# Performance work log

Hardware: AMD Instinct MI355X
Metric: run time of the kernel (lower is better)

## Reference

```python
import jax, jax.numpy as jnp
import numpy as np

NB, NL, V, VOCAB, D, TOPK = 16, 64, 16384, 32000, 256, 16
NITER, EARLY, RW = 8, 2, 0.8


def setup_inputs():
    key = jax.random.key(0)
    ks = jax.random.split(key, 8)
    probas = jax.random.uniform(ks[0], (NB, NL, V), dtype=jnp.float32) + 1e-6
    h_d = jax.random.normal(ks[1], (NB, NL, D), dtype=jnp.float32)
    lengths = jax.random.randint(ks[2], (NB,), NL // 2, NL + 1)
    mask = (jnp.arange(NL)[None, :] < lengths[:, None]).astype(jnp.int32)  # prefix mask
    batch_vocab = jax.random.randint(ks[3], (V,), 0, VOCAB)
    emb_table = jax.random.normal(ks[4], (VOCAB, D), dtype=jnp.float32) * 0.02
    W1 = jax.random.normal(ks[5], (2 * D, D), dtype=jnp.float32) * 0.006
    b1 = jnp.zeros((D,), dtype=jnp.float32)
    return {"probas": probas, "h_d": h_d, "mask": mask, "batch_vocab": batch_vocab,
            "emb_table": emb_table, "W1": W1, "b1": b1}


def _forward(probas, h_d, mask, batch_vocab, emb_table, W1, b1):
    maskf = mask.astype(probas.dtype)
    MAP = jnp.argmax(probas, axis=-1)                       # [nb,nl]
    topk_vals, topk_idx = jax.lax.top_k(probas, TOPK)       # [nb,nl,K]
    topk_vals = jnp.where(mask[..., None] < 1, 1.0, topk_vals)
    logits = jnp.log(topk_vals)                             # Categorical(probs) == categorical(log p)
    sLens = jnp.sum(mask, axis=1)                           # [nb]
    one_hot = jnp.arange(NL)[None, :] == (sLens - 1)[:, None]  # one_hot_by_mask: last valid pos
    m2d = (mask[:, :, None] * mask[:, None, :]) > 0
    eyeM = jnp.eye(NL, dtype=probas.dtype)
    h_masked = h_d * maskf[..., None]

    def step(carry, k):
        max_score, best, count, stopped = carry
        choice = jax.random.categorical(k, logits)          # [nb,nl]
        samples = jnp.take_along_axis(topk_idx, choice[..., None], axis=-1)[..., 0]
        samples = jnp.where(one_hot, MAP, samples)
        embs = emb_table[batch_vocab[samples]] * maskf[..., None]   # gather+embed, masked
        new_embs = jax.nn.relu(jnp.concatenate([embs, h_masked], axis=-1) @ W1 + b1)
        Kmat = jnp.einsum('bld,bmd->blm', new_embs, new_embs)       # [nb,nl,nl]
        # det of leading lxl submatrix == det with padded rows/cols replaced by identity
        score = jnp.linalg.det(jnp.where(m2d, Kmat, eyeM))          # [nb]
        improved = score > max_score
        any_imp = jnp.any(improved)
        count = jnp.where(any_imp, 0, count + 1)
        upd = improved & (~stopped)
        stopped = stopped | ((~any_imp) & (count >= EARLY))
        max_score = jnp.where(upd, score, max_score)
        best = jnp.where(upd[:, None], samples, best)
        return (max_score, best, count, stopped), None

    init = (jnp.full((NB,), -jnp.inf, probas.dtype), MAP, jnp.int32(0), jnp.bool_(False))
    keys = jax.random.split(jax.random.key(42), NITER)
    (max_score, best, _, _), _ = jax.lax.scan(step, init, keys)

    # diverse_proba: scatter redist_weight at best choice, (1-rw) elsewhere, renormalize
    am = jnp.where(jnp.arange(V)[None, None, :] == best[:, :, None], RW, 1.0 - RW).astype(probas.dtype)
    x = probas * am
    nm = jnp.sum(x, axis=-1, keepdims=True)
    nm = jnp.where(maskf[..., None] == 0, 1e-10, nm)
    return x / nm, max_score


def reference(probas, h_d, mask, batch_vocab, emb_table, W1, b1):
    return _forward(probas, h_d, mask, batch_vocab, emb_table, W1, b1)
```

## Files before the change

### kernel.cpp

```cpp
#include <hip/hip_runtime.h>
#include <math.h>
#include <stdint.h>


#define TINYF 1.17549435082228750797e-38f

#define KMX(r, c) (((r) * 68) + ((c) ^ ((((r) >> 3) & 7) << 2)))

struct Keys16 { uint32_t k[16]; };

__host__ __device__ inline void tf2x32(uint32_t k0, uint32_t k1,
                                       uint32_t x0, uint32_t x1,
                                       uint32_t* o0, uint32_t* o1) {
  uint32_t ks2 = k0 ^ k1 ^ 0x1BD11BDAu;
  uint32_t ks[3] = {k0, k1, ks2};
  uint32_t v0 = x0 + k0, v1 = x1 + k1;
  const int R0[4] = {13, 15, 26, 6};
  const int R1[4] = {17, 29, 16, 24};
#pragma unroll
  for (int g = 0; g < 5; ++g) {
    const int* RR = (g & 1) ? R1 : R0;
#pragma unroll
    for (int r = 0; r < 4; ++r) {
      v0 += v1;
      v1 = (v1 << RR[r]) | (v1 >> (32 - RR[r]));
      v1 ^= v0;
    }
    v0 += ks[(g + 1) % 3];
    v1 += ks[(g + 2) % 3] + (uint32_t)(g + 1);
  }
  *o0 = v0; *o1 = v1;
}

__device__ inline float logf_ref(float x) { return (float)log((double)x); }

__device__ inline void wsync() {
  asm volatile("s_waitcnt lgkmcnt(0)" ::: "memory");
  __builtin_amdgcn_sched_barrier(0);
}

__device__ inline unsigned long long u64max(unsigned long long a,
                                            unsigned long long b) {
  return (a > b) ? a : b;
}

__global__ __launch_bounds__(256) void k_topk(const float* __restrict__ probas,
                                              const int* __restrict__ mask,
                                              int* __restrict__ topk_idx,
                                              float* __restrict__ logits,
                                              float* __restrict__ S) {
  int row = blockIdx.x;
  int t = threadIdx.x;
  const float* p = probas + (size_t)row * 16384;
  __shared__ unsigned long long lists[256][16];
  __shared__ float swsum[4];
  __shared__ int lcnt;
  unsigned long long* cand = &lists[0][0];

  cand[t] = 0ull;
  cand[t + 256] = 0ull;
  if (t == 0) lcnt = 0;
  __syncthreads();

  const uint32_t TB = 0x3F7E0000u;
  float sum = 0.f;
  const float4* p4 = (const float4*)p;
#pragma unroll 4
  for (int j = 0; j < 16; ++j) {
    float4 x = p4[t + j * 256];
    int v0 = (t + j * 256) * 4;
    uint32_t u0 = __float_as_uint(x.x), u1 = __float_as_uint(x.y);
    uint32_t u2 = __float_as_uint(x.z), u3 = __float_as_uint(x.w);
    sum += x.x; sum += x.y; sum += x.z; sum += x.w;
    uint32_t um = max(max(u0, u1), max(u2, u3));
    if (um >= TB) {
      if (u0 >= TB) { int s = atomicAdd(&lcnt, 1); if (s < 512)
          cand[s] = ((unsigned long long)u0 << 32) | (unsigned)(~(v0 + 0)); }
      if (u1 >= TB) { int s = atomicAdd(&lcnt, 1); if (s < 512)
          cand[s] = ((unsigned long long)u1 << 32) | (unsigned)(~(v0 + 1)); }
      if (u2 >= TB) { int s = atomicAdd(&lcnt, 1); if (s < 512)
          cand[s] = ((unsigned long long)u2 << 32) | (unsigned)(~(v0 + 2)); }
      if (u3 >= TB) { int s = atomicAdd(&lcnt, 1); if (s < 512)
          cand[s] = ((unsigned long long)u3 << 32) | (unsigned)(~(v0 + 3)); }
    }
  }
#pragma unroll
  for (int off = 32; off >= 1; off >>= 1) sum += __shfl_down(sum, off);
  if ((t & 63) == 0) swsum[t >> 6] = sum;
  __syncthreads();
  if (t == 0) S[row] = ((swsum[0] + swsum[1]) + swsum[2]) + swsum[3];

  int n = lcnt;
  if (n >= 16 && n <= 512) {
    if (t < 64) {
      unsigned long long c[8];
#pragma unroll
      for (int k = 0; k < 8; ++k) c[k] = cand[t + 64 * k];
      unsigned long long win = 0ull;
#pragma unroll
      for (int r = 0; r < 16; ++r) {
        unsigned long long m = c[0];
#pragma unroll
        for (int k = 1; k < 8; ++k) m = u64max(m, c[k]);
#pragma unroll
        for (int off = 32; off >= 1; off >>= 1) {
          unsigned long long o = __shfl_xor(m, off);
          m = u64max(m, o);
        }
        if (t == r) win = m;
#pragma unroll
        for (int k = 0; k < 8; ++k) if (c[k] == m) c[k] = 0ull;
      }
      if (t < 16) {
        int idx = (int)(~(unsigned)(win & 0xFFFFFFFFull));
        float val = __uint_as_float((unsigned)(win >> 32));
        topk_idx[row * 16 + t] = idx;
        logits[row * 16 + t] = (mask[row] == 0) ? 0.0f : logf_ref(val);
      }
    }
    return;
  }

  {
    unsigned long long loc[16];
#pragma unroll
    for (int q = 0; q < 16; ++q) loc[q] = 0ull;
    for (int j = 0; j < 64; ++j) {
      int v = t + j * 256;
      float x = p[v];
      unsigned long long key =
          ((unsigned long long)__float_as_uint(x) << 32) | (unsigned)(~v);
      if (key > loc[15]) {
        loc[15] = key;
#pragma unroll
        for (int q = 15; q > 0; --q) {
          if (loc[q] > loc[q - 1]) {
            unsigned long long tmp = loc[q]; loc[q] = loc[q - 1]; loc[q - 1] = tmp;
          }
        }
      }
    }
    __syncthreads();
#pragma unroll
    for (int q = 0; q < 16; ++q) lists[t][q] = loc[q];
    __syncthreads();
    for (int nl = 128; nl >= 1; nl >>= 1) {
      if (t < nl) {
        unsigned long long M[16];
        int ia = 0, ib = 0;
#pragma unroll
        for (int q = 0; q < 16; ++q) {
          unsigned long long av = lists[t][ia];
          unsigned long long bv = lists[t + nl][ib];
          if (av >= bv) { M[q] = av; ia++; } else { M[q] = bv; ib++; }
        }
#pragma unroll
        for (int q = 0; q < 16; ++q) lists[t][q] = M[q];
      }
      __syncthreads();
    }
    if (t < 16) {
      unsigned long long key = lists[0][t];
      int idx = (int)(~(unsigned)(key & 0xFFFFFFFFull));
      float val = __uint_as_float((unsigned)(key >> 32));
      topk_idx[row * 16 + t] = idx;
      logits[row * 16 + t] = (mask[row] == 0) ? 0.0f : logf_ref(val);
    }
  }
}

__global__ __launch_bounds__(256) void k_sample(Keys16 keys,
                                                const int* __restrict__ mask,
                                                const int* __restrict__ topk_idx,
                                                const float* __restrict__ logits,
                                                int* __restrict__ samples,
                                                int* __restrict__ choice) {
  int tid = blockIdx.x * 256 + threadIdx.x;
  int i = tid >> 10;
  int rbl = tid & 1023;
  int b = rbl >> 6;
  int l = rbl & 63;
  uint32_t k0 = keys.k[2 * i], k1 = keys.k[2 * i + 1];
  int sl = 0;
  for (int m = 0; m < 64; ++m) sl += mask[b * 64 + m];
  float bestv = 0.f; int bestk = 0;
#pragma unroll
  for (int k = 0; k < 16; ++k) {
    uint32_t j = (uint32_t)((b * 64 + l) * 16 + k);
    uint32_t y0, y1;
    tf2x32(k0, k1, 0u, j, &y0, &y1);
    uint32_t bits = y0 ^ y1;
    float f = __uint_as_float((bits >> 9) | 0x3f800000u) - 1.0f;
    float u = fmaxf(TINYF, f * 1.0f + TINYF);
    float t1 = logf_ref(u);
    float g = -logf_ref(-t1);
    float sv = g + logits[rbl * 16 + k];
    if (k == 0 || sv > bestv) { bestv = sv; bestk = k; }
  }
  int ce = (l == sl - 1) ? 0 : bestk;
  choice[tid] = ce;
  samples[tid] = topk_idx[rbl * 16 + ce];
}

__global__ __launch_bounds__(256) void k_ce(const int* __restrict__ topk_idx,
                                            const int* __restrict__ batch_vocab,
                                            const float* __restrict__ emb,
                                            const float* __restrict__ W1,
                                            const float* __restrict__ h_d,
                                            const float* __restrict__ b1,
                                            const int* __restrict__ mask,
                                            float* __restrict__ Eall) {
  int row = blockIdx.x;
  int t = threadIdx.x;
  __shared__ int rid[16];
  __shared__ float e[16][256];
  __shared__ float hl[256];
  float mkf = (float)mask[row];
  if (t < 16) rid[t] = batch_vocab[topk_idx[row * 16 + t]];
  hl[t] = h_d[(size_t)row * 256 + t] * mkf;
  __syncthreads();
#pragma unroll
  for (int k = 0; k < 16; ++k) e[k][t] = emb[(size_t)rid[k] * 256 + t];
  __syncthreads();
  float acch = 0.f;
  for (int j0 = 0; j0 < 256; j0 += 4) {
    float4 hv = *(const float4*)&hl[j0];
    float w0 = W1[(256 + j0 + 0) * 256 + t];
    float w1 = W1[(256 + j0 + 1) * 256 + t];
    float w2 = W1[(256 + j0 + 2) * 256 + t];
    float w3 = W1[(256 + j0 + 3) * 256 + t];
    acch = fmaf(hv.x, w0, acch);
    acch = fmaf(hv.y, w1, acch);
    acch = fmaf(hv.z, w2, acch);
    acch = fmaf(hv.w, w3, acch);
  }
  float acc[16];
#pragma unroll
  for (int k = 0; k < 16; ++k) acc[k] = 0.f;
  for (int j0 = 0; j0 < 256; j0 += 4) {
    float w0 = W1[(j0 + 0) * 256 + t];
    float w1 = W1[(j0 + 1) * 256 + t];
    float w2 = W1[(j0 + 2) * 256 + t];
    float w3 = W1[(j0 + 3) * 256 + t];
#pragma unroll
    for (int k = 0; k < 16; ++k) {
      float4 ev = *(const float4*)&e[k][j0];
      acc[k] = fmaf(ev.x, w0, acc[k]);
      acc[k] = fmaf(ev.y, w1, acc[k]);
      acc[k] = fmaf(ev.z, w2, acc[k]);
      acc[k] = fmaf(ev.w, w3, acc[k]);
    }
  }
  float b1v = b1[t];
#pragma unroll
  for (int k = 0; k < 16; ++k) {
    float val = fmaf(mkf, acc[k], acch) + b1v;
    Eall[((size_t)row * 16 + k) * 256 + t] = fmaxf(val, 0.0f);
  }
}

__global__ __launch_bounds__(256) void k_gram(const float* __restrict__ Eall,
                                              const int* __restrict__ mask,
                                              const int* __restrict__ choice,
                                              float* __restrict__ scores) {
  int blk = blockIdx.x;
  int i = blk >> 4, b = blk & 15;
  int t = threadIdx.x;
  __shared__ __align__(16) float Ett[64][68];
  __shared__ __align__(16) float KmF[64 * 68];
  __shared__ int ch[64];
  int mskv = 0;
  if (t < 64) {
    ch[t] = choice[i * 1024 + b * 64 + t];
    mskv = mask[b * 64 + t];
  }
  __syncthreads();
  int l = t & 63, wd = t >> 6;
  const float* eptr =
      Eall + ((size_t)((b * 64 + l) * 16 + ch[l])) * 256 + wd * 16;
  float acc[16];
#pragma unroll
  for (int q = 0; q < 16; ++q) acc[q] = 0.f;
  int tx = t & 15, ty = t >> 4;
  for (int dt = 0; dt < 4; ++dt) {
    const float* src = eptr + dt * 64;
    float4 v0 = *(const float4*)(src + 0);
    float4 v1 = *(const float4*)(src + 4);
    float4 v2 = *(const float4*)(src + 8);
    float4 v3 = *(const float4*)(src + 12);
    int d0 = wd * 16;
    Ett[d0 +  0][l] = v0.x; Ett[d0 +  1][l] = v0.y;
    Ett[d0 +  2][l] = v0.z; Ett[d0 +  3][l] = v0.w;
    Ett[d0 +  4][l] = v1.x; Ett[d0 +  5][l] = v1.y;
    Ett[d0 +  6][l] = v1.z; Ett[d0 +  7][l] = v1.w;
    Ett[d0 +  8][l] = v2.x; Ett[d0 +  9][l] = v2.y;
    Ett[d0 + 10][l] = v2.z; Ett[d0 + 11][l] = v2.w;
    Ett[d0 + 12][l] = v3.x; Ett[d0 + 13][l] = v3.y;
    Ett[d0 + 14][l] = v3.z; Ett[d0 + 15][l] = v3.w;
    __syncthreads();
#pragma unroll 4
    for (int dd = 0; dd < 64; ++dd) {
      float4 av4 = *(const float4*)&Ett[dd][tx * 4];
      float4 bv4 = *(const float4*)&Ett[dd][ty * 4];
      float avv[4] = {av4.x, av4.y, av4.z, av4.w};
      float bvv[4] = {bv4.x, bv4.y, bv4.z, bv4.w};
#pragma unroll
      for (int a2 = 0; a2 < 4; ++a2)
#pragma unroll
        for (int c2 = 0; c2 < 4; ++c2)
          acc[a2 * 4 + c2] = fmaf(avv[a2], bvv[c2], acc[a2 * 4 + c2]);
    }
    __syncthreads();
  }
#pragma unroll
  for (int a2 = 0; a2 < 4; ++a2)
#pragma unroll
    for (int c2 = 0; c2 < 4; ++c2)
      KmF[KMX(tx * 4 + a2, ty * 4 + c2)] = acc[a2 * 4 + c2];
  __syncthreads();
  if (t >= 64) return;

  unsigned long long bal = __ballot(mskv != 0);
  int L = __popcll(bal);

  float sdet = 1.f, ssign = 1.f;
  int pos = t;
  float curcol = KmF[KMX(t, 0)];

  for (int p = 0; p < L; ++p) {
    bool cnd = (pos >= p) && (pos < L);
    unsigned lo = (((unsigned)(63 - pos)) << 6) | (unsigned)t;
    unsigned long long key =
        cnd ? ((((unsigned long long)__float_as_uint(fabsf(curcol))) << 32) | lo)
            : 0ull;
#pragma unroll
    for (int off = 32; off >= 1; off >>= 1) {
      unsigned long long o = __shfl_xor(key, off);
      if (o > key) key = o;
    }
    int lane_rb = (int)(key & 63u);
    int pb = 63 - (int)((key >> 6) & 63u);
    float kpp = __shfl(curcol, lane_rb);
    sdet *= kpp;
    if (pb != p) ssign = -ssign;
    int np = pos;
    if (pos == p) np = pb;
    if (t == lane_rb) np = p;
    pos = np;
    bool active = (pos > p) && (pos < L);
    if (active) {
      float f = (kpp != 0.f) ? (curcol / kpp) : 0.f;
      float nf = -f;
      int c0 = (p + 1) & ~3;
      int sel = (p + 1) & 3;
      for (int c = c0; c < L; c += 4) {
        float4 pr = *(const float4*)&KmF[KMX(lane_rb, c)];
        float4 tr = *(float4*)&KmF[KMX(t, c)];
        tr.x = fmaf(nf, pr.x, tr.x);
        tr.y = fmaf(nf, pr.y, tr.y);
        tr.z = fmaf(nf, pr.z, tr.z);
        tr.w = fmaf(nf, pr.w, tr.w);
        *(float4*)&KmF[KMX(t, c)] = tr;
        if (c == c0) {
          curcol = (sel == 0) ? tr.x : (sel == 1) ? tr.y
                 : (sel == 2) ? tr.z : tr.w;
        }
      }
    }
    wsync();
  }
  if (t == 0) scores[i * 16 + b] = sdet * ssign;
}

__global__ void k_select(const float* __restrict__ scores,
                         int* __restrict__ win,
                         float* __restrict__ out_ms) {
  if (threadIdx.x == 0 && blockIdx.x == 0) {
    float ms[16]; int w[16];
    for (int b = 0; b < 16; ++b) { ms[b] = -INFINITY; w[b] = -1; }
    int count = 0; bool stopped = false;
    for (int i = 0; i < 8; ++i) {
      bool any = false; bool imp[16];
      for (int b = 0; b < 16; ++b) {
        imp[b] = scores[i * 16 + b] > ms[b];
        any = any || imp[b];
      }
      count = any ? 0 : (count + 1);
      for (int b = 0; b < 16; ++b) {
        if (imp[b] && !stopped) { ms[b] = scores[i * 16 + b]; w[b] = i; }
      }
      stopped = stopped || ((!any) && (count >= 2));
    }
    for (int b = 0; b < 16; ++b) { win[b] = w[b]; out_ms[b] = ms[b]; }
  }
}

__global__ __launch_bounds__(256) void k_out(const float* __restrict__ probas,
                                             const int* __restrict__ mask,
                                             const int* __restrict__ samples,
                                             const int* __restrict__ topk_idx,
                                             const int* __restrict__ win,
                                             const float* __restrict__ S,
                                             float* __restrict__ out) {
  int row = blockIdx.x;
  int b = row >> 6;
  int t = threadIdx.x;
  int wi = win[b];
  int best = (wi >= 0) ? samples[wi * 1024 + row] : topk_idx[row * 16];
  const float* p = probas + (size_t)row * 16384;
  float* o = out + (size_t)row * 16384;
  float nm;
  if (mask[row] == 0) {
    nm = 1e-10f;
  } else {
    nm = 0.2f * S[row] + 0.6f * p[best];
  }
  const float4* p4 = (const float4*)p;
  float4* o4 = (float4*)o;
  for (int f = t; f < 4096; f += 256) {
    float4 x = p4[f];
    int v0 = f << 2;
    float4 r;
    r.x = x.x * ((v0 + 0 == best) ? 0.8f : 0.2f) / nm;
    r.y = x.y * ((v0 + 1 == best) ? 0.8f : 0.2f) / nm;
    r.z = x.z * ((v0 + 2 == best) ? 0.8f : 0.2f) / nm;
    r.w = x.w * ((v0 + 3 == best) ? 0.8f : 0.2f) / nm;
    o4[f] = r;
  }
}

extern "C" void kernel_launch(void* const* d_in, const int* in_sizes, int n_in,
                              void* d_out, int out_size, void* d_ws, size_t ws_size,
                              hipStream_t stream) {
  const float* probas = (const float*)d_in[0];
  const float* h_d    = (const float*)d_in[1];
  const int*   mask   = (const int*)d_in[2];
  const int*   bvoc   = (const int*)d_in[3];
  const float* emb    = (const float*)d_in[4];
  const float* W1     = (const float*)d_in[5];
  const float* b1     = (const float*)d_in[6];
  float* out = (float*)d_out;

  char* w = (char*)d_ws;
  int*   topk_idx = (int*)w;   w += 16384 * sizeof(int);
  float* logits   = (float*)w; w += 16384 * sizeof(float);
  float* S        = (float*)w; w += 1024 * sizeof(float);
  int*   samples  = (int*)w;   w += 8192 * sizeof(int);
  int*   choice   = (int*)w;   w += 8192 * sizeof(int);
  float* scores   = (float*)w; w += 128 * sizeof(float);
  int*   win      = (int*)w;   w += 16 * sizeof(int);

  float* Eall = out;

  Keys16 keys;
  for (uint32_t i = 0; i < 8; ++i) {
    uint32_t a, bq;
    tf2x32(0u, 42u, 0u, i, &a, &bq);
    keys.k[2 * i] = a; keys.k[2 * i + 1] = bq;
  }

  k_topk<<<1024, 256, 0, stream>>>(probas, mask, topk_idx, logits, S);
  k_sample<<<32, 256, 0, stream>>>(keys, mask, topk_idx, logits, samples, choice);
  k_ce<<<1024, 256, 0, stream>>>(topk_idx, bvoc, emb, W1, h_d, b1, mask, Eall);
  k_gram<<<128, 256, 0, stream>>>(Eall, mask, choice, scores);
  k_select<<<1, 64, 0, stream>>>(scores, win, out + 16777216);
  k_out<<<1024, 256, 0, stream>>>(probas, mask, samples, topk_idx, win, S, out);
}
```

Before: 314.5 us.

## Keep determinant rows in registers with readlane broadcasts; fold select into output kernel

The LU elimination in k_gram now keeps each lane's 64-element row of the Gram matrix in registers. It broadcasts pivot-row values with readlane instead of doing float4 LDS reads, writes and waitcnt syncs on every pivot step, which removes LDS traffic from the serial determinant loop. The tiny single-thread k_select kernel is removed: every k_out block now recomputes the early-stopping selection from the 128 scores, saving one launch. The trade-offs are a fully unrolled 64-step loop with high register pressure (launch bounds set to one block), and redundant selection work repeated in all 1024 output blocks.

New measurement: 306.4 us. 1.03x faster.

```diff
diff --git a/kernel.cpp b/kernel.cpp
--- a/kernel.cpp
+++ b/kernel.cpp
@@ -34,14 +34,14 @@
 
 __device__ inline float logf_ref(float x) { return (float)log((double)x); }
 
-__device__ inline void wsync() {
-  asm volatile("s_waitcnt lgkmcnt(0)" ::: "memory");
-  __builtin_amdgcn_sched_barrier(0);
-}
-
 __device__ inline unsigned long long u64max(unsigned long long a,
                                             unsigned long long b) {
   return (a > b) ? a : b;
+}
+
+__device__ inline float lane_bcast_f32(float v, int slane) {
+  return __uint_as_float(
+      (unsigned)__builtin_amdgcn_readlane(__float_as_int(v), slane));
 }
 
 __global__ __launch_bounds__(256) void k_topk(const float* __restrict__ probas,
@@ -259,10 +259,10 @@
   }
 }
 
-__global__ __launch_bounds__(256) void k_gram(const float* __restrict__ Eall,
-                                              const int* __restrict__ mask,
-                                              const int* __restrict__ choice,
-                                              float* __restrict__ scores) {
+__global__ __launch_bounds__(256, 1) void k_gram(const float* __restrict__ Eall,
+                                                 const int* __restrict__ mask,
+                                                 const int* __restrict__ choice,
+                                                 float* __restrict__ scores) {
   int blk = blockIdx.x;
   int i = blk >> 4, b = blk & 15;
   int t = threadIdx.x;
@@ -323,89 +323,93 @@
   unsigned long long bal = __ballot(mskv != 0);
   int L = __popcll(bal);
 
+  float km[64];
+#pragma unroll
+  for (int c0 = 0; c0 < 64; c0 += 4) {
+    float4 v = *(const float4*)&KmF[KMX(t, c0)];
+    km[c0 + 0] = v.x; km[c0 + 1] = v.y; km[c0 + 2] = v.z; km[c0 + 3] = v.w;
+  }
+
   float sdet = 1.f, ssign = 1.f;
   int pos = t;
-  float curcol = KmF[KMX(t, 0)];
-
-  for (int p = 0; p < L; ++p) {
-    bool cnd = (pos >= p) && (pos < L);
-    unsigned lo = (((unsigned)(63 - pos)) << 6) | (unsigned)t;
-    unsigned long long key =
-        cnd ? ((((unsigned long long)__float_as_uint(fabsf(curcol))) << 32) | lo)
-            : 0ull;
-#pragma unroll
-    for (int off = 32; off >= 1; off >>= 1) {
-      unsigned long long o = __shfl_xor(key, off);
-      if (o > key) key = o;
-    }
-    int lane_rb = (int)(key & 63u);
-    int pb = 63 - (int)((key >> 6) & 63u);
-    float kpp = __shfl(curcol, lane_rb);
-    sdet *= kpp;
-    if (pb != p) ssign = -ssign;
-    int np = pos;
-    if (pos == p) np = pb;
-    if (t == lane_rb) np = p;
-    pos = np;
-    bool active = (pos > p) && (pos < L);
-    if (active) {
-      float f = (kpp != 0.f) ? (curcol / kpp) : 0.f;
+
+#pragma unroll
+  for (int p = 0; p < 64; ++p) {
+    if (p < L) {
+      bool cnd = (pos >= p) && (pos < L);
+      unsigned lo = (((unsigned)(63 - pos)) << 6) | (unsigned)t;
+      unsigned long long key =
+          cnd ? ((((unsigned long long)__float_as_uint(fabsf(km[p]))) << 32) | lo)
+              : 0ull;
+#pragma unroll
+      for (int off = 32; off >= 1; off >>= 1) {
+        unsigned long long o = __shfl_xor(key, off);
+        if (o > key) key = o;
+      }
+      int lane_rb = (int)(key & 63u);
+      int pb = 63 - (int)((key >> 6) & 63u);
+      int srb = __builtin_amdgcn_readfirstlane(lane_rb);
+      float kpp = lane_bcast_f32(km[p], srb);
+      sdet *= kpp;
+      if (pb != p) ssign = -ssign;
+      int np = pos;
+      if (pos == p) np = pb;
+      if (t == lane_rb) np = p;
+      pos = np;
+      bool active = (pos > p) && (pos < L);
+      float f = (active && kpp != 0.f) ? (km[p] / kpp) : 0.f;
       float nf = -f;
-      int c0 = (p + 1) & ~3;
-      int sel = (p + 1) & 3;
-      for (int c = c0; c < L; c += 4) {
-        float4 pr = *(const float4*)&KmF[KMX(lane_rb, c)];
-        float4 tr = *(float4*)&KmF[KMX(t, c)];
-        tr.x = fmaf(nf, pr.x, tr.x);
-        tr.y = fmaf(nf, pr.y, tr.y);
-        tr.z = fmaf(nf, pr.z, tr.z);
-        tr.w = fmaf(nf, pr.w, tr.w);
-        *(float4*)&KmF[KMX(t, c)] = tr;
-        if (c == c0) {
-          curcol = (sel == 0) ? tr.x : (sel == 1) ? tr.y
-                 : (sel == 2) ? tr.z : tr.w;
-        }
-      }
-    }
-    wsync();
+#pragma unroll
+      for (int c = p + 1; c < 64; ++c) {
+        float pr = lane_bcast_f32(km[c], srb);
+        if (active) km[c] = fmaf(nf, pr, km[c]);
+      }
+    }
   }
   if (t == 0) scores[i * 16 + b] = sdet * ssign;
-}
-
-__global__ void k_select(const float* __restrict__ scores,
-                         int* __restrict__ win,
-                         float* __restrict__ out_ms) {
-  if (threadIdx.x == 0 && blockIdx.x == 0) {
-    float ms[16]; int w[16];
-    for (int b = 0; b < 16; ++b) { ms[b] = -INFINITY; w[b] = -1; }
-    int count = 0; bool stopped = false;
-    for (int i = 0; i < 8; ++i) {
-      bool any = false; bool imp[16];
-      for (int b = 0; b < 16; ++b) {
-        imp[b] = scores[i * 16 + b] > ms[b];
-        any = any || imp[b];
-      }
-      count = any ? 0 : (count + 1);
-      for (int b = 0; b < 16; ++b) {
-        if (imp[b] && !stopped) { ms[b] = scores[i * 16 + b]; w[b] = i; }
-      }
-      stopped = stopped || ((!any) && (count >= 2));
-    }
-    for (int b = 0; b < 16; ++b) { win[b] = w[b]; out_ms[b] = ms[b]; }
-  }
 }
 
 __global__ __launch_bounds__(256) void k_out(const float* __restrict__ probas,
                                              const int* __restrict__ mask,
                                              const int* __restrict__ samples,
                                              const int* __restrict__ topk_idx,
-                                             const int* __restrict__ win,
+                                             const float* __restrict__ scores,
                                              const float* __restrict__ S,
-                                             float* __restrict__ out) {
+                                             float* __restrict__ out,
+                                             float* __restrict__ out_ms) {
   int row = blockIdx.x;
   int b = row >> 6;
   int t = threadIdx.x;
-  int wi = win[b];
+  __shared__ float ssc[128];
+  if (t < 128) ssc[t] = scores[t];
+  __syncthreads();
+  float ms[16]; int w[16];
+#pragma unroll
+  for (int q = 0; q < 16; ++q) { ms[q] = -INFINITY; w[q] = -1; }
+  int count = 0; bool stopped = false;
+#pragma unroll
+  for (int i = 0; i < 8; ++i) {
+    bool any = false; bool imp[16];
+#pragma unroll
+    for (int q = 0; q < 16; ++q) {
+      imp[q] = ssc[i * 16 + q] > ms[q];
+      any = any || imp[q];
+    }
+    count = any ? 0 : (count + 1);
+#pragma unroll
+    for (int q = 0; q < 16; ++q) {
+      if (imp[q] && !stopped) { ms[q] = ssc[i * 16 + q]; w[q] = i; }
+    }
+    stopped = stopped || ((!any) && (count >= 2));
+  }
+  if (row == 0 && t == 0) {
+#pragma unroll
+    for (int q = 0; q < 16; ++q) out_ms[q] = ms[q];
+  }
+  int wi = -1;
+#pragma unroll
+  for (int q = 0; q < 16; ++q) if (b == q) wi = w[q];
+
   int best = (wi >= 0) ? samples[wi * 1024 + row] : topk_idx[row * 16];
   const float* p = probas + (size_t)row * 16384;
   float* o = out + (size_t)row * 16384;
@@ -448,7 +452,6 @@
   int*   samples  = (int*)w;   w += 8192 * sizeof(int);
   int*   choice   = (int*)w;   w += 8192 * sizeof(int);
   float* scores   = (float*)w; w += 128 * sizeof(float);
-  int*   win      = (int*)w;   w += 16 * sizeof(int);
 
   float* Eall = out;
 
@@ -463,6 +466,6 @@
   k_sample<<<32, 256, 0, stream>>>(keys, mask, topk_idx, logits, samples, choice);
   k_ce<<<1024, 256, 0, stream>>>(topk_idx, bvoc, emb, W1, h_d, b1, mask, Eall);
   k_gram<<<128, 256, 0, stream>>>(Eall, mask, choice, scores);
-  k_select<<<1, 64, 0, stream>>>(scores, win, out + 16777216);
-  k_out<<<1024, 256, 0, stream>>>(probas, mask, samples, topk_idx, win, S, out);
-}
+  k_out<<<1024, 256, 0, stream>>>(probas, mask, samples, topk_idx, scores, S,
+                                  out, out + 16777216);
+}
```
